# Optimization experiments

Hardware: AMD Instinct MI355X
Metric: run time of the kernel (lower is better)

The kernel has to match this reference:

```python
import jax, jax.numpy as jnp
import numpy as np

N_NODES = 20000
N_GRAPH = 256
NODE_DIM = 128
MULS = (128, 64, 32)       # node irreps: 128x0e + 64x1o + 32x2e
HC = 32                    # hidden channels per irrep
HIDDEN_DIM = 64
N_PATH = 9                 # feasible uuw paths into 0e+1e+2e
W_NUMEL = N_PATH * HC * HC # 9216


def _tables():
    # real Clebsch-Gordan tensors built from cartesian tensor algebra,
    # normalized so that sum(C**2) = 2*l_out + 1 (component normalization)
    eps = np.zeros((3, 3, 3))
    eps[0, 1, 2] = eps[1, 2, 0] = eps[2, 0, 1] = 1.0
    eps[0, 2, 1] = eps[2, 1, 0] = eps[1, 0, 2] = -1.0
    s2, s6 = 1 / np.sqrt(2), 1 / np.sqrt(6)
    Q2 = np.zeros((5, 3, 3))  # orthonormal basis of traceless symmetric 3x3
    Q2[0, 0, 1] = Q2[0, 1, 0] = s2          # xy
    Q2[1, 1, 2] = Q2[1, 2, 1] = s2          # yz
    Q2[2, 0, 0] = Q2[2, 1, 1] = -s6; Q2[2, 2, 2] = 2 * s6  # z2
    Q2[3, 0, 2] = Q2[3, 2, 0] = s2          # xz
    Q2[4, 0, 0] = s2; Q2[4, 1, 1] = -s2     # x2-y2

    def nrm(C, l3):
        return C * np.sqrt((2 * l3 + 1) / (C ** 2).sum())

    C000 = np.ones((1, 1, 1))
    C022 = np.eye(5)[None, :, :]
    C110 = np.eye(3).reshape(3, 3, 1) / np.sqrt(3)
    C111 = eps / np.sqrt(2)
    C112 = np.transpose(Q2, (1, 2, 0))
    C202 = np.eye(5)[:, None, :]
    C220 = np.eye(5).reshape(5, 5, 1) / np.sqrt(5)
    M = np.einsum('iab,jdb->ijad', Q2, Q2)  # [5,5,3,3]
    C221 = nrm(np.einsum('cad,ijad->ijc', eps, M), 1)
    S = 0.5 * (M + np.transpose(M, (0, 1, 3, 2)))
    S = S - np.trace(S, axis1=2, axis2=3)[..., None, None] * np.eye(3) / 3.0
    C222 = nrm(np.einsum('kad,ijad->ijk', Q2, S), 2)
    # sph2cart change of basis: 9 spherical comps (0e+1e+2e) -> 3x3 cartesian
    Qc = np.zeros((3, 3, 9))
    Qc[:, :, 0] = np.eye(3) / np.sqrt(3)        # isotropic part
    Qc[:, :, 1:4] = eps / np.sqrt(2)            # antisymmetric part
    Qc[:, :, 4:9] = np.transpose(Q2, (1, 2, 0)) # symmetric traceless part
    return [C000, C022, C110, C111, C112, C202, C220, C221, C222], Qc

_CGS, _QC = _tables()


def setup_inputs() -> dict:
    key = jax.random.key(0)
    ks = jax.random.split(key, 12)
    f32 = jnp.float32
    d_sph = MULS[0] + 3 * MULS[1] + 5 * MULS[2]  # 480
    return {
        'x_scalar': jax.random.normal(ks[0], (N_NODES, NODE_DIM), f32),
        'x_spherical': jax.random.normal(ks[1], (N_NODES, d_sph), f32),
        'batch': jnp.sort(jax.random.randint(ks[2], (N_NODES,), 0, N_GRAPH)),
        'W0e': jax.random.normal(ks[3], (MULS[0], HC), f32),
        'W1o': jax.random.normal(ks[4], (MULS[1], HC), f32),
        'W2e': jax.random.normal(ks[5], (MULS[2], HC), f32),
        'Wm1': jax.random.normal(ks[6], (NODE_DIM, HIDDEN_DIM), f32) / np.sqrt(NODE_DIM),
        'bm1': jnp.zeros((HIDDEN_DIM,), f32),
        'Wm2': jax.random.normal(ks[7], (HIDDEN_DIM, W_NUMEL), f32) / np.sqrt(HIDDEN_DIM),
        'bm2': jnp.zeros((W_NUMEL,), f32),
        'P0': jax.random.normal(ks[8], (3 * HC,), f32),
        'P1': jax.random.normal(ks[9], (2 * HC,), f32),
        'P2': jax.random.normal(ks[10], (4 * HC,), f32),
    }


def reference(x_scalar, x_spherical, batch, W0e, W1o, W2e, Wm1, bm1, Wm2, bm2, P0, P1, P2):
    n = x_scalar.shape[0]
    m0, m1, m2 = MULS
    # split node features into irrep blocks
    x0 = x_spherical[:, :m0, None]                        # [N,128,1] 0e
    x1 = x_spherical[:, m0:m0 + 3 * m1].reshape(n, m1, 3) # [N,64,3]  1o
    x2 = x_spherical[:, m0 + 3 * m1:].reshape(n, m2, 5)   # [N,32,5]  2e
    # pre_lin: per-irrep channel mixing (e3nn-style 1/sqrt(fan_in))
    h = [jnp.einsum('num,uv->nvm', x, W) / np.sqrt(W.shape[0])
         for x, W in ((x0, W0e), (x1, W1o), (x2, W2e))]   # each [N,32,2l+1]
    # per-node tensor-product weights from scalar features
    w = (jax.nn.silu(x_scalar @ Wm1 + bm1) @ Wm2 + bm2).reshape(n, N_PATH, HC, HC)
    # uuw tensor product, path order matches _CGS
    paths = ((0, 0), (0, 2), (1, 1), (1, 1), (1, 1), (2, 0), (2, 2), (2, 2), (2, 2))
    inv_u = 1.0 / np.sqrt(HC)
    outs = []
    for k, (i, j) in enumerate(paths):
        C = jnp.asarray(_CGS[k], x_scalar.dtype)
        outs.append(jnp.einsum('pqr,nup,nuq,nuw->nwr', C, h[i], h[j], w[:, k]) * inv_u)
    # post_lin: combine paths of each output l into a single channel
    y0 = jnp.einsum('num,u->nm', jnp.concatenate([outs[0], outs[2], outs[6]], 1), P0) / np.sqrt(3 * HC)
    y1 = jnp.einsum('num,u->nm', jnp.concatenate([outs[3], outs[7]], 1), P1) / np.sqrt(2 * HC)
    y2 = jnp.einsum('num,u->nm', jnp.concatenate([outs[1], outs[4], outs[5], outs[8]], 1), P2) / np.sqrt(4 * HC)
    sph = jnp.concatenate([y0, y1, y2], axis=1)           # [N,9]
    cart = jnp.einsum('abi,ni->nab', jnp.asarray(_QC, sph.dtype), sph)  # [N,3,3]
    red = jax.ops.segment_sum(cart, batch, num_segments=N_GRAPH)        # [B,3,3]
    # if_trace is False (if_iso=False): roll every non-batch dim by 1
    return jnp.roll(jnp.roll(red, 1, axis=1), 1, axis=2)
```

## Files before the change

### kernel.cpp

```cpp
#include <hip/hip_runtime.h>
#include <math.h>

#define OFF_W2P 0
#define OFF_B2P 14336
#define OFF_V   14560
#define WS_FLOATS 4494560

#define SC_Y0 0.0180421959121758f
#define SC_Y2 0.015625f
#define S2f 0.70710678118654752f
#define S6f 0.40824829046386302f
#define TWOS2f 1.41421356237309505f
#define TWOS6f 0.81649658092772603f
#define ISQRT3 0.57735026918962576f
#define ISQRT5 0.44721359549995794f
#define H0SC 0.08838834764831845f
#define H1SC 0.125f
#define H2SC 0.17677669529663689f

__device__ __constant__ int KARR[7] = {0, 1, 2, 4, 5, 6, 8};

__global__ __launch_bounds__(256) void prep_kernel(
    const float* __restrict__ Wm2, const float* __restrict__ bm2,
    const float* __restrict__ P0, const float* __restrict__ P2,
    float* __restrict__ ws, float* __restrict__ out) {
  int j = blockIdx.x * 256 + threadIdx.x;
  if (j < 2304) out[j] = 0.f;

  if (j < 14336) {
    int s = j >> 11; int rem = j & 2047; int c = rem >> 5; int u = rem & 31;
    int k = KARR[s];
    const float* P;
    float sc;
    switch (s) {
      case 0: P = P0;      sc = SC_Y0; break;
      case 1: P = P2;      sc = SC_Y2; break;
      case 2: P = P0 + 32; sc = SC_Y0; break;
      case 3: P = P2 + 32; sc = SC_Y2; break;
      case 4: P = P2 + 64; sc = SC_Y2; break;
      case 5: P = P0 + 64; sc = SC_Y0; break;
      default: P = P2 + 96; sc = SC_Y2; break;
    }
    const float4* w4 = (const float4*)(Wm2 + c * 9216 + k * 1024 + u * 32);
    const float4* p4 = (const float4*)P;
    float acc = 0.f;
#pragma unroll
    for (int q = 0; q < 8; ++q) {
      float4 a = w4[q], b = p4[q];
      acc += a.x * b.x + a.y * b.y + a.z * b.z + a.w * b.w;
    }
    ws[OFF_W2P + c * 224 + s * 32 + u] = acc * sc;
  } else if (j < 14560) {
    int i = j - 14336; int s = i >> 5; int u = i & 31; int k = KARR[s];
    const float* P;
    float sc;
    switch (s) {
      case 0: P = P0;      sc = SC_Y0; break;
      case 1: P = P2;      sc = SC_Y2; break;
      case 2: P = P0 + 32; sc = SC_Y0; break;
      case 3: P = P2 + 32; sc = SC_Y2; break;
      case 4: P = P2 + 64; sc = SC_Y2; break;
      case 5: P = P0 + 64; sc = SC_Y0; break;
      default: P = P2 + 96; sc = SC_Y2; break;
    }
    const float* b = bm2 + k * 1024 + u * 32;
    float acc = 0.f;
#pragma unroll
    for (int w = 0; w < 32; ++w) acc += b[w] * P[w];
    ws[OFF_B2P + s * 32 + u] = acc * sc;
  }
}

__global__ __launch_bounds__(256) void kv_kernel(
    const float* __restrict__ xs_g, const float* __restrict__ Wm1,
    const float* __restrict__ bm1, float* __restrict__ ws) {
  __shared__ __align__(16) float xs[16][132];
  __shared__ float hiT[64][19];
  const int tid = threadIdx.x;
  const int n0 = blockIdx.x * 16;

  for (int idx = tid; idx < 512; idx += 256) {
    const int row = idx >> 5, c4 = idx & 31;
    *(float4*)&xs[row][c4 * 4] = *(const float4*)(xs_g + (n0 + row) * 128 + c4 * 4);
  }
  __syncthreads();

  {
    const int n = tid >> 4, c0 = (tid & 15) * 4;
    float acc[4] = {0.f, 0.f, 0.f, 0.f};
#pragma unroll 4
    for (int mq = 0; mq < 32; ++mq) {
      const float4 xv = *(float4*)&xs[n][mq * 4];
      const float xa[4] = {xv.x, xv.y, xv.z, xv.w};
#pragma unroll
      for (int r = 0; r < 4; ++r) {
        const float4 w = *(const float4*)(Wm1 + (mq * 4 + r) * 64 + c0);
        acc[0] += xa[r] * w.x; acc[1] += xa[r] * w.y;
        acc[2] += xa[r] * w.z; acc[3] += xa[r] * w.w;
      }
    }
    const float4 bb = *(const float4*)(bm1 + c0);
    const float bv[4] = {bb.x, bb.y, bb.z, bb.w};
#pragma unroll
    for (int jj = 0; jj < 4; ++jj) {
      float z = acc[jj] + bv[jj];
      hiT[c0 + jj][n] = z / (1.f + __expf(-z));
    }
  }
  __syncthreads();

  if (tid < 224) {
    const int og = tid >> 3, ng = tid & 7;
    const int o0 = og * 8, n = ng * 2;
    const float4 blo = *(const float4*)(ws + OFF_B2P + o0);
    const float4 bhi = *(const float4*)(ws + OFF_B2P + o0 + 4);
    float acc[2][8];
#pragma unroll
    for (int i = 0; i < 2; ++i) {
      acc[i][0] = blo.x; acc[i][1] = blo.y; acc[i][2] = blo.z; acc[i][3] = blo.w;
      acc[i][4] = bhi.x; acc[i][5] = bhi.y; acc[i][6] = bhi.z; acc[i][7] = bhi.w;
    }
#pragma unroll 2
    for (int c = 0; c < 64; ++c) {
      const float h0v = hiT[c][n], h1v = hiT[c][n + 1];
      const float4 wlo = *(const float4*)(ws + OFF_W2P + c * 224 + o0);
      const float4 whi = *(const float4*)(ws + OFF_W2P + c * 224 + o0 + 4);
      const float wv[8] = {wlo.x, wlo.y, wlo.z, wlo.w, whi.x, whi.y, whi.z, whi.w};
#pragma unroll
      for (int jj = 0; jj < 8; ++jj) {
        acc[0][jj] += h0v * wv[jj];
        acc[1][jj] += h1v * wv[jj];
      }
    }
#pragma unroll
    for (int i = 0; i < 2; ++i) {
      const int n_g = n0 + n + i;
      float4 a = {acc[i][0], acc[i][1], acc[i][2], acc[i][3]};
      float4 b = {acc[i][4], acc[i][5], acc[i][6], acc[i][7]};
      *(float4*)(ws + OFF_V + n_g * 224 + o0) = a;
      *(float4*)(ws + OFF_V + n_g * 224 + o0 + 4) = b;
    }
  }
}

__global__ __launch_bounds__(256) void khd_kernel(
    const float* __restrict__ xsph, const int* __restrict__ batch,
    const float* __restrict__ W0e, const float* __restrict__ W1o,
    const float* __restrict__ W2e,
    const float* __restrict__ ws, float* __restrict__ out, const float norm2) {
  __shared__ __align__(16) char smem[33216];
  float (*Vs)[224]     = (float (*)[224])smem;
  float (*h0s)[32]     = (float (*)[32])(smem + 14336);
  float (*h1s)[3][32]  = (float (*)[3][32])(smem + 16384);
  float (*h2s)[5][32]  = (float (*)[5][32])(smem + 22528);
  float (*sphs)[6]     = (float (*)[6])(smem + 32768);
  int* batch_s         = (int*)(smem + 33152);

  const int tid = threadIdx.x;
  const int n0 = blockIdx.x * 16;

  if (tid < 16) batch_s[tid] = batch[n0 + tid];

  if (tid < 64) {
    const int n = tid & 15, ug = tid >> 4, u0 = ug * 8;
    const float4* x4 = (const float4*)(xsph + (size_t)(n0 + n) * 480);
    float acc[8] = {0.f, 0.f, 0.f, 0.f, 0.f, 0.f, 0.f, 0.f};
#pragma unroll 4
    for (int mq = 0; mq < 32; ++mq) {
      const float4 xv = x4[mq];
      const float xa[4] = {xv.x, xv.y, xv.z, xv.w};
#pragma unroll
      for (int r = 0; r < 4; ++r) {
        const float4 wl = *(const float4*)(W0e + (mq * 4 + r) * 32 + u0);
        const float4 wh = *(const float4*)(W0e + (mq * 4 + r) * 32 + u0 + 4);
        const float xr = xa[r];
        acc[0] += xr * wl.x; acc[1] += xr * wl.y; acc[2] += xr * wl.z; acc[3] += xr * wl.w;
        acc[4] += xr * wh.x; acc[5] += xr * wh.y; acc[6] += xr * wh.z; acc[7] += xr * wh.w;
      }
    }
    float4 a = {acc[0] * H0SC, acc[1] * H0SC, acc[2] * H0SC, acc[3] * H0SC};
    float4 b = {acc[4] * H0SC, acc[5] * H0SC, acc[6] * H0SC, acc[7] * H0SC};
    *(float4*)&h0s[n][u0] = a;
    *(float4*)&h0s[n][u0 + 4] = b;
  } else if (tid < 128) {
    const int t = tid - 64;
    const int n = t & 15, ug = t >> 4, u0 = ug * 8;
    const float4* x4 = (const float4*)(xsph + (size_t)(n0 + n) * 480);
    float acc[3][8] = {{0.f}};
#pragma unroll 2
    for (int mq = 0; mq < 16; ++mq) {
      const float4 a0 = x4[32 + mq * 3];
      const float4 a1 = x4[32 + mq * 3 + 1];
      const float4 a2 = x4[32 + mq * 3 + 2];
      const float xa[12] = {a0.x, a0.y, a0.z, a0.w, a1.x, a1.y, a1.z, a1.w,
                            a2.x, a2.y, a2.z, a2.w};
#pragma unroll
      for (int mm = 0; mm < 4; ++mm) {
        const float4 wl = *(const float4*)(W1o + (mq * 4 + mm) * 32 + u0);
        const float4 wh = *(const float4*)(W1o + (mq * 4 + mm) * 32 + u0 + 4);
        const float wv[8] = {wl.x, wl.y, wl.z, wl.w, wh.x, wh.y, wh.z, wh.w};
#pragma unroll
        for (int j = 0; j < 3; ++j) {
          const float xr = xa[mm * 3 + j];
#pragma unroll
          for (int jj = 0; jj < 8; ++jj) acc[j][jj] += xr * wv[jj];
        }
      }
    }
#pragma unroll
    for (int j = 0; j < 3; ++j) {
      float4 a = {acc[j][0] * H1SC, acc[j][1] * H1SC, acc[j][2] * H1SC, acc[j][3] * H1SC};
      float4 b = {acc[j][4] * H1SC, acc[j][5] * H1SC, acc[j][6] * H1SC, acc[j][7] * H1SC};
      *(float4*)&h1s[n][j][u0] = a;
      *(float4*)&h1s[n][j][u0 + 4] = b;
    }
  } else if (tid < 192) {
    const int t = tid - 128;
    const int n = t & 15, ug = t >> 4, u0 = ug * 8;
    const float4* x4 = (const float4*)(xsph + (size_t)(n0 + n) * 480);
    float acc[5][8] = {{0.f}};
#pragma unroll 2
    for (int mq = 0; mq < 8; ++mq) {
      const float4 a0 = x4[80 + mq * 5];
      const float4 a1 = x4[80 + mq * 5 + 1];
      const float4 a2 = x4[80 + mq * 5 + 2];
      const float4 a3 = x4[80 + mq * 5 + 3];
      const float4 a4 = x4[80 + mq * 5 + 4];
      const float xa[20] = {a0.x, a0.y, a0.z, a0.w, a1.x, a1.y, a1.z, a1.w,
                            a2.x, a2.y, a2.z, a2.w, a3.x, a3.y, a3.z, a3.w,
                            a4.x, a4.y, a4.z, a4.w};
#pragma unroll
      for (int mm = 0; mm < 4; ++mm) {
        const float4 wl = *(const float4*)(W2e + (mq * 4 + mm) * 32 + u0);
        const float4 wh = *(const float4*)(W2e + (mq * 4 + mm) * 32 + u0 + 4);
        const float wv[8] = {wl.x, wl.y, wl.z, wl.w, wh.x, wh.y, wh.z, wh.w};
#pragma unroll
        for (int j = 0; j < 5; ++j) {
          const float xr = xa[mm * 5 + j];
#pragma unroll
          for (int jj = 0; jj < 8; ++jj) acc[j][jj] += xr * wv[jj];
        }
      }
    }
#pragma unroll
    for (int j = 0; j < 5; ++j) {
      float4 a = {acc[j][0] * H2SC, acc[j][1] * H2SC, acc[j][2] * H2SC, acc[j][3] * H2SC};
      float4 b = {acc[j][4] * H2SC, acc[j][5] * H2SC, acc[j][6] * H2SC, acc[j][7] * H2SC};
      *(float4*)&h2s[n][j][u0] = a;
      *(float4*)&h2s[n][j][u0 + 4] = b;
    }
  } else {
    const int t = tid - 192;
    const float* Vg = ws + OFF_V + (size_t)n0 * 224;
#pragma unroll
    for (int q = 0; q < 14; ++q) {
      const int idx = t + q * 64;
      const int n = idx / 56, o4 = idx % 56;
      *(float4*)&Vs[n][o4 * 4] = *(const float4*)(Vg + n * 224 + o4 * 4);
    }
  }
  __syncthreads();

  {
    const int nl = tid >> 5, u = tid & 31;
#pragma unroll 2
    for (int half = 0; half < 2; ++half) {
      const int n = half * 8 + nl;
      const float h0 = h0s[n][u];
      const float h1a = h1s[n][0][u], h1b = h1s[n][1][u], h1c = h1s[n][2][u];
      float h2v[5];
#pragma unroll
      for (int j = 0; j < 5; ++j) h2v[j] = h2s[n][j][u];
      const float v0 = Vs[n][u],       v1 = Vs[n][u + 32],
                  v2 = Vs[n][u + 64],  v3 = Vs[n][u + 96],
                  v4 = Vs[n][u + 128], v5 = Vs[n][u + 160],
                  v6 = Vs[n][u + 192];

      const float d11 = h1a * h1a + h1b * h1b + h1c * h1c;
      const float d22 = h2v[0] * h2v[0] + h2v[1] * h2v[1] + h2v[2] * h2v[2] +
                        h2v[3] * h2v[3] + h2v[4] * h2v[4];
      float y0 = v0 * h0 * h0 + v2 * d11 * ISQRT3 + v5 * d22 * ISQRT5;

      const float o00 = h1a * h1a, o01 = h1a * h1b, o02 = h1a * h1c;
      const float o11 = h1b * h1b, o12 = h1b * h1c, o22 = h1c * h1c;
      const float t40 = TWOS2f * o01, t41 = TWOS2f * o12;
      const float t42 = S6f * (2.f * o22 - o00 - o11);
      const float t43 = TWOS2f * o02, t44 = S2f * (o00 - o11);

      const float A00 = -S6f * h2v[2] + S2f * h2v[4];
      const float A01 = S2f * h2v[0];
      const float A02 = S2f * h2v[3];
      const float A11 = -S6f * h2v[2] - S2f * h2v[4];
      const float A12 = S2f * h2v[1];
      const float A22 = TWOS6f * h2v[2];
      const float B00 = A00 * A00 + A01 * A01 + A02 * A02;
      const float B01 = A00 * A01 + A01 * A11 + A02 * A12;
      const float B02 = A00 * A02 + A01 * A12 + A02 * A22;
      const float B11 = A01 * A01 + A11 * A11 + A12 * A12;
      const float B12 = A01 * A02 + A11 * A12 + A12 * A22;
      const float B22 = A02 * A02 + A12 * A12 + A22 * A22;
      const float t80 = TWOS2f * B01, t81 = TWOS2f * B12;
      const float t82 = S6f * (2.f * B22 - B00 - B11);
      const float t83 = TWOS2f * B02, t84 = S2f * (B00 - B11);

      const float w15 = (v1 + v4) * h0;
      const float v6n = v6 * norm2;
      float y2r[5];
      y2r[0] = w15 * h2v[0] + v3 * t40 + v6n * t80;
      y2r[1] = w15 * h2v[1] + v3 * t41 + v6n * t81;
      y2r[2] = w15 * h2v[2] + v3 * t42 + v6n * t82;
      y2r[3] = w15 * h2v[3] + v3 * t43 + v6n * t83;
      y2r[4] = w15 * h2v[4] + v3 * t44 + v6n * t84;

#pragma unroll
      for (int off = 16; off > 0; off >>= 1) {
        y0 += __shfl_xor(y0, off, 32);
#pragma unroll
        for (int r = 0; r < 5; ++r) y2r[r] += __shfl_xor(y2r[r], off, 32);
      }
      if (u == 0) {
        sphs[n][0] = y0;
#pragma unroll
        for (int r = 0; r < 5; ++r) sphs[n][1 + r] = y2r[r];
      }
    }
  }
  __syncthreads();

  if (tid < 9) {
    const float QW[9][6] = {
        {ISQRT3, 0.f, 0.f, -S6f, 0.f, S2f},
        {0.f, S2f, 0.f, 0.f, 0.f, 0.f},
        {0.f, 0.f, 0.f, 0.f, S2f, 0.f},
        {0.f, S2f, 0.f, 0.f, 0.f, 0.f},
        {ISQRT3, 0.f, 0.f, -S6f, 0.f, -S2f},
        {0.f, 0.f, S2f, 0.f, 0.f, 0.f},
        {0.f, 0.f, 0.f, 0.f, S2f, 0.f},
        {0.f, 0.f, S2f, 0.f, 0.f, 0.f},
        {ISQRT3, 0.f, 0.f, TWOS6f, 0.f, 0.f}};
    const int a = tid / 3, b = tid % 3;
    const int rolled = ((a + 1) % 3) * 3 + ((b + 1) % 3);
    const float c0 = QW[tid][0], c1 = QW[tid][1], c2 = QW[tid][2];
    const float c3 = QW[tid][3], c4 = QW[tid][4], c5 = QW[tid][5];
    int cur_g = batch_s[0];
    float acc = 0.f;
#pragma unroll 4
    for (int q = 0; q < 16; ++q) {
      const int g = batch_s[q];
      const float val = c0 * sphs[q][0] + c1 * sphs[q][1] + c2 * sphs[q][2] +
                        c3 * sphs[q][3] + c4 * sphs[q][4] + c5 * sphs[q][5];
      if (g != cur_g) {
        atomicAdd(out + cur_g * 9 + rolled, acc);
        acc = 0.f;
        cur_g = g;
      }
      acc += val;
    }
    atomicAdd(out + cur_g * 9 + rolled, acc);
  }
}

extern "C" void kernel_launch(void* const* d_in, const int* in_sizes, int n_in,
                              void* d_out, int out_size, void* d_ws, size_t ws_size,
                              hipStream_t stream) {
  const float* x_scalar = (const float*)d_in[0];
  const float* x_sph    = (const float*)d_in[1];
  const int*   batch    = (const int*)d_in[2];
  const float* W0e      = (const float*)d_in[3];
  const float* W1o      = (const float*)d_in[4];
  const float* W2e      = (const float*)d_in[5];
  const float* Wm1      = (const float*)d_in[6];
  const float* bm1      = (const float*)d_in[7];
  const float* Wm2      = (const float*)d_in[8];
  const float* bm2      = (const float*)d_in[9];
  const float* P0       = (const float*)d_in[10];
  const float* P2       = (const float*)d_in[12];
  float* ws  = (float*)d_ws;
  float* out = (float*)d_out;

  if (ws_size < (size_t)WS_FLOATS * sizeof(float)) return;

  double Q2[5][3][3] = {};
  const double s2d = 0.70710678118654752440, s6d = 0.40824829046386301637;
  Q2[0][0][1] = Q2[0][1][0] = s2d;
  Q2[1][1][2] = Q2[1][2][1] = s2d;
  Q2[2][0][0] = Q2[2][1][1] = -s6d; Q2[2][2][2] = 2.0 * s6d;
  Q2[3][0][2] = Q2[3][2][0] = s2d;
  Q2[4][0][0] = s2d; Q2[4][1][1] = -s2d;
  double ss = 0.0;
  for (int i = 0; i < 5; ++i)
    for (int jj = 0; jj < 5; ++jj) {
      double S[3][3];
      for (int a = 0; a < 3; ++a)
        for (int d = 0; d < 3; ++d) {
          double m1 = 0, m2 = 0;
          for (int b = 0; b < 3; ++b) {
            m1 += Q2[i][a][b] * Q2[jj][d][b];
            m2 += Q2[i][d][b] * Q2[jj][a][b];
          }
          S[a][d] = 0.5 * (m1 + m2);
        }
      double tr = (S[0][0] + S[1][1] + S[2][2]) / 3.0;
      S[0][0] -= tr; S[1][1] -= tr; S[2][2] -= tr;
      for (int kk = 0; kk < 5; ++kk) {
        double cc = 0;
        for (int a = 0; a < 3; ++a)
          for (int d = 0; d < 3; ++d) cc += Q2[kk][a][d] * S[a][d];
        ss += cc * cc;
      }
    }
  const float norm2 = (float)sqrt(5.0 / ss);

  prep_kernel<<<57, 256, 0, stream>>>(Wm2, bm2, P0, P2, ws, out);
  kv_kernel<<<1250, 256, 0, stream>>>(x_scalar, Wm1, bm1, ws);
  khd_kernel<<<1250, 256, 0, stream>>>(x_sph, batch, W0e, W1o, W2e, ws, out, norm2);
}
```

Measured before the change: 182.6 us.

## Rebalance khd_kernel: 8 nodes per block, staged x in LDS, balanced thread roles

The khd kernel now handles 8 nodes per block instead of 16, doubling the grid. Each block first stages the x_spherical rows into padded shared memory with coalesced float4 loads. The projection work is redistributed so all four 64-thread groups do similar amounts of FMA instead of one group doing the heavy l=2 projection. V is loaded straight into registers rather than through shared memory. This is meant to remove the load imbalance and uncoalesced per-thread global reads, at the cost of an extra barrier and twice as many atomics to the output.

```diff
diff --git a/kernel.cpp b/kernel.cpp
--- a/kernel.cpp
+++ b/kernel.cpp
@@ -148,181 +148,209 @@
     const float* __restrict__ W0e, const float* __restrict__ W1o,
     const float* __restrict__ W2e,
     const float* __restrict__ ws, float* __restrict__ out, const float norm2) {
-  __shared__ __align__(16) char smem[33216];
-  float (*Vs)[224]     = (float (*)[224])smem;
-  float (*h0s)[32]     = (float (*)[32])(smem + 14336);
-  float (*h1s)[3][32]  = (float (*)[3][32])(smem + 16384);
-  float (*h2s)[5][32]  = (float (*)[5][32])(smem + 22528);
-  float (*sphs)[6]     = (float (*)[6])(smem + 32768);
-  int* batch_s         = (int*)(smem + 33152);
+  __shared__ __align__(16) char smem[26080];
+  float (*xp)[484]    = (float (*)[484])smem;
+  float (*h0s)[36]    = (float (*)[36])(smem + 15488);
+  float (*h1s)[3][36] = (float (*)[3][36])(smem + 16640);
+  float (*h2s)[5][36] = (float (*)[5][36])(smem + 20096);
+  float (*sphs)[6]    = (float (*)[6])(smem + 25856);
+  int* batch_s        = (int*)(smem + 26048);
 
   const int tid = threadIdx.x;
-  const int n0 = blockIdx.x * 16;
-
-  if (tid < 16) batch_s[tid] = batch[n0 + tid];
+  const int n0 = blockIdx.x * 8;
+
+  const int nl = tid >> 5, u = tid & 31;
+  const float* Vg = ws + OFF_V + (size_t)(n0 + nl) * 224 + u;
+  const float v0 = Vg[0],   v1 = Vg[32],  v2 = Vg[64],  v3 = Vg[96];
+  const float v4 = Vg[128], v5 = Vg[160], v6 = Vg[192];
+
+  if (tid < 8) batch_s[tid] = batch[n0 + tid];
+
+  for (int idx = tid; idx < 960; idx += 256) {
+    const int row = idx / 120, c4 = idx % 120;
+    *(float4*)&xp[row][c4 * 4] =
+        *(const float4*)(xsph + (size_t)(n0 + row) * 480 + c4 * 4);
+  }
+  __syncthreads();
 
   if (tid < 64) {
-    const int n = tid & 15, ug = tid >> 4, u0 = ug * 8;
-    const float4* x4 = (const float4*)(xsph + (size_t)(n0 + n) * 480);
-    float acc[8] = {0.f, 0.f, 0.f, 0.f, 0.f, 0.f, 0.f, 0.f};
-#pragma unroll 4
-    for (int mq = 0; mq < 32; ++mq) {
-      const float4 xv = x4[mq];
-      const float xa[4] = {xv.x, xv.y, xv.z, xv.w};
-#pragma unroll
-      for (int r = 0; r < 4; ++r) {
-        const float4 wl = *(const float4*)(W0e + (mq * 4 + r) * 32 + u0);
-        const float4 wh = *(const float4*)(W0e + (mq * 4 + r) * 32 + u0 + 4);
-        const float xr = xa[r];
-        acc[0] += xr * wl.x; acc[1] += xr * wl.y; acc[2] += xr * wl.z; acc[3] += xr * wl.w;
-        acc[4] += xr * wh.x; acc[5] += xr * wh.y; acc[6] += xr * wh.z; acc[7] += xr * wh.w;
-      }
-    }
-    float4 a = {acc[0] * H0SC, acc[1] * H0SC, acc[2] * H0SC, acc[3] * H0SC};
-    float4 b = {acc[4] * H0SC, acc[5] * H0SC, acc[6] * H0SC, acc[7] * H0SC};
-    *(float4*)&h0s[n][u0] = a;
-    *(float4*)&h0s[n][u0 + 4] = b;
+    const int n = tid & 7, u0 = ((tid >> 3) & 7) * 4;
+    float acc[2][4] = {{0.f}};
+#pragma unroll 2
+    for (int mq = 0; mq < 16; ++mq) {
+      const float4 a0 = *(float4*)&xp[n][128 + mq * 12];
+      const float4 a1 = *(float4*)&xp[n][128 + mq * 12 + 4];
+      const float4 a2 = *(float4*)&xp[n][128 + mq * 12 + 8];
+      const float xa[12] = {a0.x, a0.y, a0.z, a0.w, a1.x, a1.y, a1.z, a1.w,
+                            a2.x, a2.y, a2.z, a2.w};
+#pragma unroll
+      for (int mm = 0; mm < 4; ++mm) {
+        const float4 w = *(const float4*)(W1o + (mq * 4 + mm) * 32 + u0);
+        const float wv[4] = {w.x, w.y, w.z, w.w};
+#pragma unroll
+        for (int j = 0; j < 2; ++j) {
+          const float xr = xa[mm * 3 + j];
+#pragma unroll
+          for (int jj = 0; jj < 4; ++jj) acc[j][jj] += xr * wv[jj];
+        }
+      }
+    }
+#pragma unroll
+    for (int j = 0; j < 2; ++j) {
+      float4 a = {acc[j][0] * H1SC, acc[j][1] * H1SC, acc[j][2] * H1SC, acc[j][3] * H1SC};
+      *(float4*)&h1s[n][j][u0] = a;
+    }
   } else if (tid < 128) {
     const int t = tid - 64;
-    const int n = t & 15, ug = t >> 4, u0 = ug * 8;
-    const float4* x4 = (const float4*)(xsph + (size_t)(n0 + n) * 480);
-    float acc[3][8] = {{0.f}};
-#pragma unroll 2
-    for (int mq = 0; mq < 16; ++mq) {
-      const float4 a0 = x4[32 + mq * 3];
-      const float4 a1 = x4[32 + mq * 3 + 1];
-      const float4 a2 = x4[32 + mq * 3 + 2];
-      const float xa[12] = {a0.x, a0.y, a0.z, a0.w, a1.x, a1.y, a1.z, a1.w,
-                            a2.x, a2.y, a2.z, a2.w};
-#pragma unroll
-      for (int mm = 0; mm < 4; ++mm) {
-        const float4 wl = *(const float4*)(W1o + (mq * 4 + mm) * 32 + u0);
-        const float4 wh = *(const float4*)(W1o + (mq * 4 + mm) * 32 + u0 + 4);
-        const float wv[8] = {wl.x, wl.y, wl.z, wl.w, wh.x, wh.y, wh.z, wh.w};
-#pragma unroll
-        for (int j = 0; j < 3; ++j) {
-          const float xr = xa[mm * 3 + j];
-#pragma unroll
-          for (int jj = 0; jj < 8; ++jj) acc[j][jj] += xr * wv[jj];
-        }
-      }
-    }
-#pragma unroll
-    for (int j = 0; j < 3; ++j) {
-      float4 a = {acc[j][0] * H1SC, acc[j][1] * H1SC, acc[j][2] * H1SC, acc[j][3] * H1SC};
-      float4 b = {acc[j][4] * H1SC, acc[j][5] * H1SC, acc[j][6] * H1SC, acc[j][7] * H1SC};
-      *(float4*)&h1s[n][j][u0] = a;
-      *(float4*)&h1s[n][j][u0 + 4] = b;
-    }
-  } else if (tid < 192) {
-    const int t = tid - 128;
-    const int n = t & 15, ug = t >> 4, u0 = ug * 8;
-    const float4* x4 = (const float4*)(xsph + (size_t)(n0 + n) * 480);
-    float acc[5][8] = {{0.f}};
+    const int n = t & 7, u0 = ((t >> 3) & 7) * 4;
+    float acc[4][4] = {{0.f}};
 #pragma unroll 2
     for (int mq = 0; mq < 8; ++mq) {
-      const float4 a0 = x4[80 + mq * 5];
-      const float4 a1 = x4[80 + mq * 5 + 1];
-      const float4 a2 = x4[80 + mq * 5 + 2];
-      const float4 a3 = x4[80 + mq * 5 + 3];
-      const float4 a4 = x4[80 + mq * 5 + 4];
+      const float4 a0 = *(float4*)&xp[n][320 + mq * 20];
+      const float4 a1 = *(float4*)&xp[n][320 + mq * 20 + 4];
+      const float4 a2 = *(float4*)&xp[n][320 + mq * 20 + 8];
+      const float4 a3 = *(float4*)&xp[n][320 + mq * 20 + 12];
+      const float4 a4 = *(float4*)&xp[n][320 + mq * 20 + 16];
       const float xa[20] = {a0.x, a0.y, a0.z, a0.w, a1.x, a1.y, a1.z, a1.w,
                             a2.x, a2.y, a2.z, a2.w, a3.x, a3.y, a3.z, a3.w,
                             a4.x, a4.y, a4.z, a4.w};
 #pragma unroll
       for (int mm = 0; mm < 4; ++mm) {
-        const float4 wl = *(const float4*)(W2e + (mq * 4 + mm) * 32 + u0);
-        const float4 wh = *(const float4*)(W2e + (mq * 4 + mm) * 32 + u0 + 4);
-        const float wv[8] = {wl.x, wl.y, wl.z, wl.w, wh.x, wh.y, wh.z, wh.w};
-#pragma unroll
-        for (int j = 0; j < 5; ++j) {
+        const float4 w = *(const float4*)(W2e + (mq * 4 + mm) * 32 + u0);
+        const float wv[4] = {w.x, w.y, w.z, w.w};
+#pragma unroll
+        for (int j = 1; j < 5; ++j) {
           const float xr = xa[mm * 5 + j];
 #pragma unroll
-          for (int jj = 0; jj < 8; ++jj) acc[j][jj] += xr * wv[jj];
+          for (int jj = 0; jj < 4; ++jj) acc[j - 1][jj] += xr * wv[jj];
         }
       }
     }
 #pragma unroll
-    for (int j = 0; j < 5; ++j) {
-      float4 a = {acc[j][0] * H2SC, acc[j][1] * H2SC, acc[j][2] * H2SC, acc[j][3] * H2SC};
-      float4 b = {acc[j][4] * H2SC, acc[j][5] * H2SC, acc[j][6] * H2SC, acc[j][7] * H2SC};
+    for (int j = 1; j < 5; ++j) {
+      float4 a = {acc[j - 1][0] * H2SC, acc[j - 1][1] * H2SC,
+                  acc[j - 1][2] * H2SC, acc[j - 1][3] * H2SC};
       *(float4*)&h2s[n][j][u0] = a;
-      *(float4*)&h2s[n][j][u0 + 4] = b;
-    }
+    }
+  } else if (tid < 192) {
+    const int t = tid - 128;
+    const int n = t & 7, u0 = ((t >> 3) & 7) * 4;
+    float acc[4] = {0.f, 0.f, 0.f, 0.f};
+#pragma unroll 4
+    for (int mq = 0; mq < 32; ++mq) {
+      const float4 xv = *(float4*)&xp[n][mq * 4];
+      const float xa[4] = {xv.x, xv.y, xv.z, xv.w};
+#pragma unroll
+      for (int r = 0; r < 4; ++r) {
+        const float4 w = *(const float4*)(W0e + (mq * 4 + r) * 32 + u0);
+        acc[0] += xa[r] * w.x; acc[1] += xa[r] * w.y;
+        acc[2] += xa[r] * w.z; acc[3] += xa[r] * w.w;
+      }
+    }
+    float4 a = {acc[0] * H0SC, acc[1] * H0SC, acc[2] * H0SC, acc[3] * H0SC};
+    *(float4*)&h0s[n][u0] = a;
   } else {
     const int t = tid - 192;
-    const float* Vg = ws + OFF_V + (size_t)n0 * 224;
-#pragma unroll
-    for (int q = 0; q < 14; ++q) {
-      const int idx = t + q * 64;
-      const int n = idx / 56, o4 = idx % 56;
-      *(float4*)&Vs[n][o4 * 4] = *(const float4*)(Vg + n * 224 + o4 * 4);
+    const int n = t & 7, u0 = ((t >> 3) & 7) * 4;
+    float acc1[4] = {0.f, 0.f, 0.f, 0.f};
+#pragma unroll 2
+    for (int mq = 0; mq < 16; ++mq) {
+      const float4 a0 = *(float4*)&xp[n][128 + mq * 12];
+      const float4 a1 = *(float4*)&xp[n][128 + mq * 12 + 4];
+      const float4 a2 = *(float4*)&xp[n][128 + mq * 12 + 8];
+      const float xa[12] = {a0.x, a0.y, a0.z, a0.w, a1.x, a1.y, a1.z, a1.w,
+                            a2.x, a2.y, a2.z, a2.w};
+#pragma unroll
+      for (int mm = 0; mm < 4; ++mm) {
+        const float4 w = *(const float4*)(W1o + (mq * 4 + mm) * 32 + u0);
+        const float xr = xa[mm * 3 + 2];
+        acc1[0] += xr * w.x; acc1[1] += xr * w.y;
+        acc1[2] += xr * w.z; acc1[3] += xr * w.w;
+      }
+    }
+    {
+      float4 a = {acc1[0] * H1SC, acc1[1] * H1SC, acc1[2] * H1SC, acc1[3] * H1SC};
+      *(float4*)&h1s[n][2][u0] = a;
+    }
+    float acc2[4] = {0.f, 0.f, 0.f, 0.f};
+#pragma unroll 2
+    for (int mq = 0; mq < 8; ++mq) {
+      const float4 a0 = *(float4*)&xp[n][320 + mq * 20];
+      const float4 a1 = *(float4*)&xp[n][320 + mq * 20 + 4];
+      const float4 a2 = *(float4*)&xp[n][320 + mq * 20 + 8];
+      const float4 a3 = *(float4*)&xp[n][320 + mq * 20 + 12];
+      const float4 a4 = *(float4*)&xp[n][320 + mq * 20 + 16];
+      const float xa[20] = {a0.x, a0.y, a0.z, a0.w, a1.x, a1.y, a1.z, a1.w,
+                            a2.x, a2.y, a2.z, a2.w, a3.x, a3.y, a3.z, a3.w,
+                            a4.x, a4.y, a4.z, a4.w};
+#pragma unroll
+      for (int mm = 0; mm < 4; ++mm) {
+        const float4 w = *(const float4*)(W2e + (mq * 4 + mm) * 32 + u0);
+        const float xr = xa[mm * 5 + 0];
+        acc2[0] += xr * w.x; acc2[1] += xr * w.y;
+        acc2[2] += xr * w.z; acc2[3] += xr * w.w;
+      }
+    }
+    {
+      float4 a = {acc2[0] * H2SC, acc2[1] * H2SC, acc2[2] * H2SC, acc2[3] * H2SC};
+      *(float4*)&h2s[n][0][u0] = a;
     }
   }
   __syncthreads();
 
   {
-    const int nl = tid >> 5, u = tid & 31;
-#pragma unroll 2
-    for (int half = 0; half < 2; ++half) {
-      const int n = half * 8 + nl;
-      const float h0 = h0s[n][u];
-      const float h1a = h1s[n][0][u], h1b = h1s[n][1][u], h1c = h1s[n][2][u];
-      float h2v[5];
-#pragma unroll
-      for (int j = 0; j < 5; ++j) h2v[j] = h2s[n][j][u];
-      const float v0 = Vs[n][u],       v1 = Vs[n][u + 32],
-                  v2 = Vs[n][u + 64],  v3 = Vs[n][u + 96],
-                  v4 = Vs[n][u + 128], v5 = Vs[n][u + 160],
-                  v6 = Vs[n][u + 192];
-
-      const float d11 = h1a * h1a + h1b * h1b + h1c * h1c;
-      const float d22 = h2v[0] * h2v[0] + h2v[1] * h2v[1] + h2v[2] * h2v[2] +
-                        h2v[3] * h2v[3] + h2v[4] * h2v[4];
-      float y0 = v0 * h0 * h0 + v2 * d11 * ISQRT3 + v5 * d22 * ISQRT5;
-
-      const float o00 = h1a * h1a, o01 = h1a * h1b, o02 = h1a * h1c;
-      const float o11 = h1b * h1b, o12 = h1b * h1c, o22 = h1c * h1c;
-      const float t40 = TWOS2f * o01, t41 = TWOS2f * o12;
-      const float t42 = S6f * (2.f * o22 - o00 - o11);
-      const float t43 = TWOS2f * o02, t44 = S2f * (o00 - o11);
-
-      const float A00 = -S6f * h2v[2] + S2f * h2v[4];
-      const float A01 = S2f * h2v[0];
-      const float A02 = S2f * h2v[3];
-      const float A11 = -S6f * h2v[2] - S2f * h2v[4];
-      const float A12 = S2f * h2v[1];
-      const float A22 = TWOS6f * h2v[2];
-      const float B00 = A00 * A00 + A01 * A01 + A02 * A02;
-      const float B01 = A00 * A01 + A01 * A11 + A02 * A12;
-      const float B02 = A00 * A02 + A01 * A12 + A02 * A22;
-      const float B11 = A01 * A01 + A11 * A11 + A12 * A12;
-      const float B12 = A01 * A02 + A11 * A12 + A12 * A22;
-      const float B22 = A02 * A02 + A12 * A12 + A22 * A22;
-      const float t80 = TWOS2f * B01, t81 = TWOS2f * B12;
-      const float t82 = S6f * (2.f * B22 - B00 - B11);
-      const float t83 = TWOS2f * B02, t84 = S2f * (B00 - B11);
-
-      const float w15 = (v1 + v4) * h0;
-      const float v6n = v6 * norm2;
-      float y2r[5];
-      y2r[0] = w15 * h2v[0] + v3 * t40 + v6n * t80;
-      y2r[1] = w15 * h2v[1] + v3 * t41 + v6n * t81;
-      y2r[2] = w15 * h2v[2] + v3 * t42 + v6n * t82;
-      y2r[3] = w15 * h2v[3] + v3 * t43 + v6n * t83;
-      y2r[4] = w15 * h2v[4] + v3 * t44 + v6n * t84;
-
-#pragma unroll
-      for (int off = 16; off > 0; off >>= 1) {
-        y0 += __shfl_xor(y0, off, 32);
-#pragma unroll
-        for (int r = 0; r < 5; ++r) y2r[r] += __shfl_xor(y2r[r], off, 32);
-      }
-      if (u == 0) {
-        sphs[n][0] = y0;
-#pragma unroll
-        for (int r = 0; r < 5; ++r) sphs[n][1 + r] = y2r[r];
-      }
+    const float h0 = h0s[nl][u];
+    const float h1a = h1s[nl][0][u], h1b = h1s[nl][1][u], h1c = h1s[nl][2][u];
+    float h2v[5];
+#pragma unroll
+    for (int j = 0; j < 5; ++j) h2v[j] = h2s[nl][j][u];
+
+    const float d11 = h1a * h1a + h1b * h1b + h1c * h1c;
+    const float d22 = h2v[0] * h2v[0] + h2v[1] * h2v[1] + h2v[2] * h2v[2] +
+                      h2v[3] * h2v[3] + h2v[4] * h2v[4];
+    float y0 = v0 * h0 * h0 + v2 * d11 * ISQRT3 + v5 * d22 * ISQRT5;
+
+    const float o00 = h1a * h1a, o01 = h1a * h1b, o02 = h1a * h1c;
+    const float o11 = h1b * h1b, o12 = h1b * h1c, o22 = h1c * h1c;
+    const float t40 = TWOS2f * o01, t41 = TWOS2f * o12;
+    const float t42 = S6f * (2.f * o22 - o00 - o11);
+    const float t43 = TWOS2f * o02, t44 = S2f * (o00 - o11);
+
+    const float A00 = -S6f * h2v[2] + S2f * h2v[4];
+    const float A01 = S2f * h2v[0];
+    const float A02 = S2f * h2v[3];
+    const float A11 = -S6f * h2v[2] - S2f * h2v[4];
+    const float A12 = S2f * h2v[1];
+    const float A22 = TWOS6f * h2v[2];
+    const float B00 = A00 * A00 + A01 * A01 + A02 * A02;
+    const float B01 = A00 * A01 + A01 * A11 + A02 * A12;
+    const float B02 = A00 * A02 + A01 * A12 + A02 * A22;
+    const float B11 = A01 * A01 + A11 * A11 + A12 * A12;
+    const float B12 = A01 * A02 + A11 * A12 + A12 * A22;
+    const float B22 = A02 * A02 + A12 * A12 + A22 * A22;
+    const float t80 = TWOS2f * B01, t81 = TWOS2f * B12;
+    const float t82 = S6f * (2.f * B22 - B00 - B11);
+    const float t83 = TWOS2f * B02, t84 = S2f * (B00 - B11);
+
+    const float w15 = (v1 + v4) * h0;
+    const float v6n = v6 * norm2;
+    float y2r[5];
+    y2r[0] = w15 * h2v[0] + v3 * t40 + v6n * t80;
+    y2r[1] = w15 * h2v[1] + v3 * t41 + v6n * t81;
+    y2r[2] = w15 * h2v[2] + v3 * t42 + v6n * t82;
+    y2r[3] = w15 * h2v[3] + v3 * t43 + v6n * t83;
+    y2r[4] = w15 * h2v[4] + v3 * t44 + v6n * t84;
+
+#pragma unroll
+    for (int off = 16; off > 0; off >>= 1) {
+      y0 += __shfl_xor(y0, off, 32);
+#pragma unroll
+      for (int r = 0; r < 5; ++r) y2r[r] += __shfl_xor(y2r[r], off, 32);
+    }
+    if (u == 0) {
+      sphs[nl][0] = y0;
+#pragma unroll
+      for (int r = 0; r < 5; ++r) sphs[nl][1 + r] = y2r[r];
     }
   }
   __syncthreads();
@@ -344,8 +372,8 @@
     const float c3 = QW[tid][3], c4 = QW[tid][4], c5 = QW[tid][5];
     int cur_g = batch_s[0];
     float acc = 0.f;
-#pragma unroll 4
-    for (int q = 0; q < 16; ++q) {
+#pragma unroll
+    for (int q = 0; q < 8; ++q) {
       const int g = batch_s[q];
       const float val = c0 * sphs[q][0] + c1 * sphs[q][1] + c2 * sphs[q][2] +
                         c3 * sphs[q][3] + c4 * sphs[q][4] + c5 * sphs[q][5];
@@ -413,5 +441,5 @@
 
   prep_kernel<<<57, 256, 0, stream>>>(Wm2, bm2, P0, P2, ws, out);
   kv_kernel<<<1250, 256, 0, stream>>>(x_scalar, Wm1, bm1, ws);
-  khd_kernel<<<1250, 256, 0, stream>>>(x_sph, batch, W0e, W1o, W2e, ws, out, norm2);
+  khd_kernel<<<2500, 256, 0, stream>>>(x_sph, batch, W0e, W1o, W2e, ws, out, norm2);
 }
```

After: 173.2 us. -5.2%, faster.
